# Performance work log

Measured on AMD Instinct MI355X. Metric: run time of the kernel, lower is better.

Reference implementation:

```python
import jax, jax.numpy as jnp
import numpy as np

B, S, D_IN = 2, 2048, 1024
D_OUT, H, W = 1024, 16, 256
HD = D_OUT // H
SCALE = 1.0 / np.sqrt(HD).astype(np.float32)


def setup_inputs() -> dict:
    key = jax.random.key(0)
    k1, k2, k3 = jax.random.split(key, 3)
    x = jax.random.normal(k1, (B, S, D_IN), dtype=jnp.float32)
    W_qkv = jax.random.normal(k2, (3 * D_OUT, D_IN), dtype=jnp.float32) * 0.02
    W_out = jax.random.normal(k3, (D_OUT, D_OUT), dtype=jnp.float32) * 0.02
    b_out = jnp.zeros((D_OUT,), dtype=jnp.float32)
    return {"x": x, "W_qkv": W_qkv, "W_out": W_out, "b_out": b_out}


def reference(x, W_qkv, W_out, b_out):
    b, s, _ = x.shape
    qkv = x @ W_qkv.T  # [b, s, 3*D_OUT]
    q, k, v = jnp.split(qkv, 3, axis=-1)
    # [b, h, s, hd]
    q = q.reshape(b, s, H, HD).transpose(0, 2, 1, 3)
    k = k.reshape(b, s, H, HD).transpose(0, 2, 1, 3)
    v = v.reshape(b, s, H, HD).transpose(0, 2, 1, 3)
    scores = jnp.einsum('bhqd,bhkd->bhqk', q, k) * SCALE
    idx = jnp.arange(s)
    mask = jnp.abs(idx[:, None] - idx[None, :]) <= W  # symmetric band
    scores = jnp.where(mask[None, None], scores, -jnp.inf)
    probs = jax.nn.softmax(scores, axis=-1)
    ctx = jnp.einsum('bhqk,bhkd->bhqd', probs, v)
    ctx = ctx.transpose(0, 2, 1, 3).reshape(b, s, D_OUT)
    return ctx @ W_out.T + b_out
```

## Files before the change

### kernel.cpp

```cpp
#include <hip/hip_runtime.h>

#define S_LEN   2048
#define N_HEAD  16
#define WINSZ   256
#define ATT_SCALE 0.125f

typedef short bf16x8 __attribute__((ext_vector_type(8)));
typedef float f32x4  __attribute__((ext_vector_type(4)));

__device__ __forceinline__ unsigned short f2bf(float f) {
    union { float f; unsigned u; } x; x.f = f;
    return (unsigned short)((x.u + 0x7FFFu + ((x.u >> 16) & 1u)) >> 16);
}

__device__ __forceinline__ void gl2lds16(const unsigned short* g, unsigned short* l) {
    __builtin_amdgcn_global_load_lds(
        (const __attribute__((address_space(1))) unsigned int*)g,
        (__attribute__((address_space(3))) unsigned int*)l, 16, 0, 0);
}

__global__ void cvt_all(const float* __restrict__ x, const float* __restrict__ wqkv,
                        const float* __restrict__ wout,
                        unsigned short* __restrict__ xb, unsigned short* __restrict__ wqkvb,
                        unsigned short* __restrict__ woutb) {
    int i = blockIdx.x * 256 + threadIdx.x;
    const float4* src; ushort4* dst; int off;
    if (i < 1048576)              { src = (const float4*)x;    dst = (ushort4*)xb;    off = i; }
    else if (i < 1048576 + 786432){ src = (const float4*)wqkv; dst = (ushort4*)wqkvb; off = i - 1048576; }
    else                          { src = (const float4*)wout; dst = (ushort4*)woutb; off = i - 1835008; }
    float4 v = src[off];
    ushort4 o;
    o.x = f2bf(v.x); o.y = f2bf(v.y); o.z = f2bf(v.z); o.w = f2bf(v.w);
    dst[off] = o;
}

template<int MODE, int BN>
__global__ __launch_bounds__(256, 3)
void gemm_bt(const unsigned short* __restrict__ A, const unsigned short* __restrict__ Bm,
             int K,
             unsigned short* __restrict__ qout, unsigned short* __restrict__ kout,
             unsigned short* __restrict__ vtout,
             float* __restrict__ Cout, const float* __restrict__ bias, int N)
{
    constexpr int NJ = BN / 32;
    __shared__ unsigned short Als[128 * 64];
    __shared__ unsigned short Bls[BN * 64];

    const int tid   = threadIdx.x;
    const int lane  = tid & 63;
    const int wave  = tid >> 6;
    const int bm    = blockIdx.y, bn = blockIdx.x;
    const int wm    = (wave >> 1) * 64;
    const int wn    = (wave & 1) * (BN / 2);
    const int col16 = lane & 15;
    const int quad  = lane >> 4;

    f32x4 acc[4][NJ];
#pragma unroll
    for (int i = 0; i < 4; ++i)
#pragma unroll
        for (int j = 0; j < NJ; ++j)
            acc[i][j] = f32x4{0.f, 0.f, 0.f, 0.f};

    const int    grow     = lane >> 3;
    const int    gchk     = (lane & 7) ^ grow;
    const size_t laneoff  = (size_t)grow * K + gchk * 8;
    const unsigned short* gA = A  + (size_t)(bm * 128) * K + laneoff;
    const unsigned short* gB = Bm + (size_t)(bn * BN)  * K + laneoff;

    for (int k0 = 0; k0 < K; k0 += 64) {
        __syncthreads();
#pragma unroll
        for (int i = 0; i < 4; ++i) {
            const int r0 = wave * 32 + i * 8;
            gl2lds16(gA + (size_t)r0 * K + k0, &Als[r0 * 64]);
        }
#pragma unroll
        for (int i = 0; i < BN / 32; ++i) {
            const int r0 = wave * (BN / 4) + i * 8;
            gl2lds16(gB + (size_t)r0 * K + k0, &Bls[r0 * 64]);
        }
        __syncthreads();

#pragma unroll
        for (int kc = 0; kc < 2; ++kc) {
            bf16x8 af[4], bfr[NJ];
            const int sw = (kc * 4 + quad) ^ (col16 & 7);
#pragma unroll
            for (int i = 0; i < 4; ++i)
                af[i]  = *(const bf16x8*)(&Als[(wm + i * 16 + col16) * 64 + sw * 8]);
#pragma unroll
            for (int j = 0; j < NJ; ++j)
                bfr[j] = *(const bf16x8*)(&Bls[(wn + j * 16 + col16) * 64 + sw * 8]);
#pragma unroll
            for (int i = 0; i < 4; ++i)
#pragma unroll
                for (int j = 0; j < NJ; ++j)
                    acc[i][j] = __builtin_amdgcn_mfma_f32_16x16x32_bf16(af[i], bfr[j], acc[i][j], 0, 0, 0);
        }
    }

    if (MODE == 0) {
        const int which = bn >> 3;
#pragma unroll
        for (int i = 0; i < 4; ++i)
#pragma unroll
            for (int j = 0; j < NJ; ++j)
#pragma unroll
                for (int r = 0; r < 4; ++r) {
                    int m = bm * 128 + wm + i * 16 + quad * 4 + r;
                    int n = bn * BN  + wn + j * 16 + col16;
                    int rem = n & 1023;
                    int h = rem >> 6, d = rem & 63;
                    int b = m >> 11, s = m & 2047;
                    unsigned short bv = f2bf(acc[i][j][r]);
                    if (which == 0)
                        qout[((size_t)(b * N_HEAD + h) * S_LEN + s) * 64 + d] = bv;
                    else if (which == 1)
                        kout[((size_t)(b * N_HEAD + h) * S_LEN + s) * 64 + d] = bv;
                    else
                        vtout[((size_t)(b * N_HEAD + h) * 64 + d) * S_LEN + s] = bv;
                }
    } else {
#pragma unroll
        for (int i = 0; i < 4; ++i)
#pragma unroll
            for (int j = 0; j < NJ; ++j)
#pragma unroll
                for (int r = 0; r < 4; ++r) {
                    int m = bm * 128 + wm + i * 16 + quad * 4 + r;
                    int n = bn * BN  + wn + j * 16 + col16;
                    Cout[(size_t)m * N + n] = acc[i][j][r] + bias[n];
                }
    }
}

__global__ __launch_bounds__(256, 2)
void attn_kernel(const unsigned short* __restrict__ Qg, const unsigned short* __restrict__ Kg,
                 const unsigned short* __restrict__ Vtg, unsigned short* __restrict__ ctx)
{
    constexpr int LD = 72;
    __shared__ unsigned short Kls[64 * LD];
    __shared__ unsigned short Vls[64 * LD];
    __shared__ unsigned short Pls[4][32 * LD];

    const int tid  = threadIdx.x;
    const int lane = tid & 63;
    const int wave = tid >> 6;
    const int col  = lane & 15;
    const int quad = lane >> 4;

    const int bh  = blockIdx.y;
    const int Q0  = blockIdx.x * 128;
    const int q0w = Q0 + wave * 32;

    const unsigned short* Qb  = Qg  + (size_t)bh * S_LEN * 64;
    const unsigned short* Kb  = Kg  + (size_t)bh * S_LEN * 64;
    const unsigned short* Vtb = Vtg + (size_t)bh * 64 * S_LEN;

    bf16x8 qa[2][2];
#pragma unroll
    for (int qf = 0; qf < 2; ++qf)
#pragma unroll
        for (int kc = 0; kc < 2; ++kc)
            qa[qf][kc] = *(const bf16x8*)(Qb + (size_t)(q0w + qf * 16 + col) * 64 + kc * 32 + quad * 8);

    f32x4 acc[2][4];
    float lsum[2][4];
#pragma unroll
    for (int qf = 0; qf < 2; ++qf)
#pragma unroll
        for (int d = 0; d < 4; ++d) {
            acc[qf][d] = f32x4{0.f, 0.f, 0.f, 0.f};
            lsum[qf][d] = 0.f;
        }

    const int srow = tid >> 2;
    const int scg  = tid & 3;

    for (int c = 0; c < 10; ++c) {
        const int kb = Q0 - WINSZ + c * 64;
        __syncthreads();
        {
            int kk = kb + srow;
            kk = kk < 0 ? 0 : (kk > S_LEN - 1 ? S_LEN - 1 : kk);
#pragma unroll
            for (int h2 = 0; h2 < 2; ++h2) {
                const int ch = scg * 8 + h2 * 32;
                *(bf16x8*)(&Kls[srow * LD + ch]) = *(const bf16x8*)(Kb + (size_t)kk * 64 + ch);
                int ss = kb + ch;
                ss = ss < 0 ? 0 : (ss > S_LEN - 8 ? S_LEN - 8 : ss);
                *(bf16x8*)(&Vls[srow * LD + ch]) = *(const bf16x8*)(Vtb + (size_t)srow * S_LEN + ss);
            }
        }
        __syncthreads();

        if (kb > q0w + 31 + WINSZ || kb + 63 < q0w - WINSZ || kb > S_LEN - 1 || kb + 63 < 0)
            continue;

        f32x4 sc[2][4];
#pragma unroll
        for (int hf = 0; hf < 4; ++hf) {
            bf16x8 kf0 = *(const bf16x8*)(&Kls[(hf * 16 + col) * LD + quad * 8]);
            bf16x8 kf1 = *(const bf16x8*)(&Kls[(hf * 16 + col) * LD + 32 + quad * 8]);
#pragma unroll
            for (int qf = 0; qf < 2; ++qf) {
                f32x4 z = f32x4{0.f, 0.f, 0.f, 0.f};
                z = __builtin_amdgcn_mfma_f32_16x16x32_bf16(qa[qf][0], kf0, z, 0, 0, 0);
                sc[qf][hf] = __builtin_amdgcn_mfma_f32_16x16x32_bf16(qa[qf][1], kf1, z, 0, 0, 0);
            }
        }

        const bool full = (kb >= q0w + 31 - WINSZ) && (kb + 63 <= q0w + WINSZ) &&
                          (kb >= 0) && (kb + 63 <= S_LEN - 1);

        float p[2][4][4];
#pragma unroll
        for (int qf = 0; qf < 2; ++qf)
#pragma unroll
            for (int hf = 0; hf < 4; ++hf) {
                const int kkey = kb + hf * 16 + col;
#pragma unroll
                for (int r = 0; r < 4; ++r) {
                    float e = __expf(fmaf(sc[qf][hf][r], ATT_SCALE, -8.0f));
                    if (!full) {
                        int q  = q0w + qf * 16 + quad * 4 + r;
                        int dq = kkey - q;
                        bool valid = (kkey >= 0) && (kkey < S_LEN) && (dq <= WINSZ) && (dq >= -WINSZ);
                        e = valid ? e : 0.f;
                    }
                    p[qf][hf][r] = e;
                    lsum[qf][r] += e;
                }
            }

        unsigned short* pw = &Pls[wave][0];
#pragma unroll
        for (int qf = 0; qf < 2; ++qf)
#pragma unroll
            for (int hf = 0; hf < 4; ++hf)
#pragma unroll
                for (int r = 0; r < 4; ++r)
                    pw[(qf * 16 + quad * 4 + r) * LD + hf * 16 + col] = f2bf(p[qf][hf][r]);
        asm volatile("s_waitcnt lgkmcnt(0)" ::: "memory");
        bf16x8 pf[2][2];
#pragma unroll
        for (int qf = 0; qf < 2; ++qf) {
            pf[qf][0] = *(const bf16x8*)(&pw[(qf * 16 + col) * LD + quad * 8]);
            pf[qf][1] = *(const bf16x8*)(&pw[(qf * 16 + col) * LD + 32 + quad * 8]);
        }

#pragma unroll
        for (int d = 0; d < 4; ++d)
#pragma unroll
            for (int kc = 0; kc < 2; ++kc) {
                bf16x8 vf = *(const bf16x8*)(&Vls[(d * 16 + col) * LD + kc * 32 + quad * 8]);
#pragma unroll
                for (int qf = 0; qf < 2; ++qf)
                    acc[qf][d] = __builtin_amdgcn_mfma_f32_16x16x32_bf16(pf[qf][kc], vf, acc[qf][d], 0, 0, 0);
            }
    }

    const int b = bh >> 4, h = bh & 15;
#pragma unroll
    for (int qf = 0; qf < 2; ++qf)
#pragma unroll
        for (int r = 0; r < 4; ++r) {
            float v = lsum[qf][r];
            v += __shfl_xor(v, 1);
            v += __shfl_xor(v, 2);
            v += __shfl_xor(v, 4);
            v += __shfl_xor(v, 8);
            float inv = 1.f / v;
            int q = q0w + qf * 16 + quad * 4 + r;
#pragma unroll
            for (int d = 0; d < 4; ++d)
                ctx[((size_t)(b * S_LEN + q)) * 1024 + h * 64 + d * 16 + col] =
                    f2bf(acc[qf][d][r] * inv);
        }
}

extern "C" void kernel_launch(void* const* d_in, const int* in_sizes, int n_in,
                              void* d_out, int out_size, void* d_ws, size_t ws_size,
                              hipStream_t stream) {
    const float* x    = (const float*)d_in[0];
    const float* Wqkv = (const float*)d_in[1];
    const float* Wout = (const float*)d_in[2];
    const float* bout = (const float*)d_in[3];
    float* out = (float*)d_out;

    char* ws = (char*)d_ws;
    unsigned short* xb    = (unsigned short*)(ws);
    unsigned short* wqkvb = (unsigned short*)(ws + 8u  * 1024 * 1024);
    unsigned short* woutb = (unsigned short*)(ws + 14u * 1024 * 1024);
    unsigned short* qb    = (unsigned short*)(ws + 16u * 1024 * 1024);
    unsigned short* kbuf  = (unsigned short*)(ws + 24u * 1024 * 1024);
    unsigned short* vtbuf = (unsigned short*)(ws + 32u * 1024 * 1024);
    unsigned short* ctxb  = (unsigned short*)(ws + 40u * 1024 * 1024);

    cvt_all<<<8192, 256, 0, stream>>>(x, Wqkv, Wout, xb, wqkvb, woutb);

    gemm_bt<0, 128><<<dim3(24, 32), 256, 0, stream>>>(xb, wqkvb, 1024, qb, kbuf, vtbuf,
                                                      nullptr, nullptr, 0);
    attn_kernel<<<dim3(16, 32), 256, 0, stream>>>(qb, kbuf, vtbuf, ctxb);
    gemm_bt<1, 64><<<dim3(16, 32), 256, 0, stream>>>(ctxb, woutb, 1024, nullptr, nullptr, nullptr,
                                                     out, bout, 1024);
}
```

Baseline: 166.0 us.

## Stage GEMM epilogues through LDS and widen attention blocks to eight waves

The QKV GEMM epilogue now writes accumulators into shared memory and then emits 16-byte coalesced stores to Q, K and transposed V. For the V part it swaps the MFMA operands so the transpose comes out of the tile naturally. The output GEMM also stages fp32 results through LDS to produce float4 stores with the bias added. The attention kernel moves to 512 threads with 16 queries per wave, loads K and V tiles directly into swizzled LDS with global_load_lds, and uses cheaper round-half-up bf16 rounding for probabilities. The changes target scattered 2-byte global stores and attention load overhead, at the cost of extra LDS traffic and barriers, and the occupancy change may not fit.

```diff
diff --git a/kernel.cpp b/kernel.cpp
--- a/kernel.cpp
+++ b/kernel.cpp
@@ -11,6 +11,10 @@
 __device__ __forceinline__ unsigned short f2bf(float f) {
     union { float f; unsigned u; } x; x.f = f;
     return (unsigned short)((x.u + 0x7FFFu + ((x.u >> 16) & 1u)) >> 16);
+}
+__device__ __forceinline__ unsigned short f2bf_rhu(float f) {
+    union { float f; unsigned u; } x; x.f = f;
+    return (unsigned short)((x.u + 0x8000u) >> 16);
 }
 
 __device__ __forceinline__ void gl2lds16(const unsigned short* g, unsigned short* l) {
@@ -43,8 +47,9 @@
              float* __restrict__ Cout, const float* __restrict__ bias, int N)
 {
     constexpr int NJ = BN / 32;
-    __shared__ unsigned short Als[128 * 64];
-    __shared__ unsigned short Bls[BN * 64];
+    __shared__ __align__(16) unsigned char smem[34816];
+    unsigned short* Als = (unsigned short*)smem;
+    unsigned short* Bls = Als + 128 * 64;
 
     const int tid   = threadIdx.x;
     const int lane  = tid & 63;
@@ -54,6 +59,7 @@
     const int wn    = (wave & 1) * (BN / 2);
     const int col16 = lane & 15;
     const int quad  = lane >> 4;
+    const bool transc = (MODE == 0) && (bn >= 16);
 
     f32x4 acc[4][NJ];
 #pragma unroll
@@ -92,57 +98,98 @@
 #pragma unroll
             for (int j = 0; j < NJ; ++j)
                 bfr[j] = *(const bf16x8*)(&Bls[(wn + j * 16 + col16) * 64 + sw * 8]);
+            if (transc) {
+#pragma unroll
+                for (int i = 0; i < 4; ++i)
+#pragma unroll
+                    for (int j = 0; j < NJ; ++j)
+                        acc[i][j] = __builtin_amdgcn_mfma_f32_16x16x32_bf16(bfr[j], af[i], acc[i][j], 0, 0, 0);
+            } else {
+#pragma unroll
+                for (int i = 0; i < 4; ++i)
+#pragma unroll
+                    for (int j = 0; j < NJ; ++j)
+                        acc[i][j] = __builtin_amdgcn_mfma_f32_16x16x32_bf16(af[i], bfr[j], acc[i][j], 0, 0, 0);
+            }
+        }
+    }
+
+    __syncthreads();
+    if (MODE == 0) {
+        unsigned short* Ct = (unsigned short*)smem;
+        if (!transc) {
 #pragma unroll
             for (int i = 0; i < 4; ++i)
 #pragma unroll
                 for (int j = 0; j < NJ; ++j)
-                    acc[i][j] = __builtin_amdgcn_mfma_f32_16x16x32_bf16(af[i], bfr[j], acc[i][j], 0, 0, 0);
+#pragma unroll
+                    for (int r = 0; r < 4; ++r)
+                        Ct[(wm + i * 16 + quad * 4 + r) * 136 + wn + j * 16 + col16] =
+                            f2bf(acc[i][j][r]);
+        } else {
+#pragma unroll
+            for (int i = 0; i < 4; ++i)
+#pragma unroll
+                for (int j = 0; j < NJ; ++j)
+#pragma unroll
+                    for (int r = 0; r < 4; ++r)
+                        Ct[(wn + j * 16 + quad * 4 + r) * 136 + wm + i * 16 + col16] =
+                            f2bf(acc[i][j][r]);
+        }
+        __syncthreads();
+        const int row  = tid >> 1;
+        const int half = tid & 1;
+        const unsigned short* src = &Ct[row * 136 + half * 64];
+        if (bn < 16) {
+            int m = bm * 128 + row;
+            int b = m >> 11, s = m & 2047;
+            int h = (bn & 7) * 2 + half;
+            unsigned short* dst = (bn < 8 ? qout : kout) +
+                                  (((size_t)(b * 16 + h) * 2048 + s) * 64);
+#pragma unroll
+            for (int c = 0; c < 8; ++c)
+                *(bf16x8*)(dst + c * 8) = *(const bf16x8*)(src + c * 8);
+        } else {
+            int h = ((bn - 16) * 128 + row) >> 6;
+            int d = row & 63;
+            int b = bm >> 4;
+            int s0 = (bm & 15) * 128 + half * 64;
+            unsigned short* dst = vtout + ((size_t)(b * 16 + h) * 64 + d) * 2048 + s0;
+#pragma unroll
+            for (int c = 0; c < 8; ++c)
+                *(bf16x8*)(dst + c * 8) = *(const bf16x8*)(src + c * 8);
+        }
+    } else {
+        float* Cf = (float*)smem;
+#pragma unroll
+        for (int i = 0; i < 4; ++i)
+#pragma unroll
+            for (int j = 0; j < NJ; ++j)
+#pragma unroll
+                for (int r = 0; r < 4; ++r)
+                    Cf[(wm + i * 16 + quad * 4 + r) * 68 + wn + j * 16 + col16] = acc[i][j][r];
+        __syncthreads();
+        const int row  = tid >> 1;
+        const int half = tid & 1;
+        int m = bm * 128 + row;
+#pragma unroll
+        for (int c = 0; c < 8; ++c) {
+            int nl = half * 32 + c * 4;
+            float4 v  = *(const float4*)&Cf[row * 68 + nl];
+            float4 bb = *(const float4*)&bias[bn * 64 + nl];
+            v.x += bb.x; v.y += bb.y; v.z += bb.z; v.w += bb.w;
+            *(float4*)&Cout[(size_t)m * N + bn * 64 + nl] = v;
         }
     }
-
-    if (MODE == 0) {
-        const int which = bn >> 3;
-#pragma unroll
-        for (int i = 0; i < 4; ++i)
-#pragma unroll
-            for (int j = 0; j < NJ; ++j)
-#pragma unroll
-                for (int r = 0; r < 4; ++r) {
-                    int m = bm * 128 + wm + i * 16 + quad * 4 + r;
-                    int n = bn * BN  + wn + j * 16 + col16;
-                    int rem = n & 1023;
-                    int h = rem >> 6, d = rem & 63;
-                    int b = m >> 11, s = m & 2047;
-                    unsigned short bv = f2bf(acc[i][j][r]);
-                    if (which == 0)
-                        qout[((size_t)(b * N_HEAD + h) * S_LEN + s) * 64 + d] = bv;
-                    else if (which == 1)
-                        kout[((size_t)(b * N_HEAD + h) * S_LEN + s) * 64 + d] = bv;
-                    else
-                        vtout[((size_t)(b * N_HEAD + h) * 64 + d) * S_LEN + s] = bv;
-                }
-    } else {
-#pragma unroll
-        for (int i = 0; i < 4; ++i)
-#pragma unroll
-            for (int j = 0; j < NJ; ++j)
-#pragma unroll
-                for (int r = 0; r < 4; ++r) {
-                    int m = bm * 128 + wm + i * 16 + quad * 4 + r;
-                    int n = bn * BN  + wn + j * 16 + col16;
-                    Cout[(size_t)m * N + n] = acc[i][j][r] + bias[n];
-                }
-    }
-}
-
-__global__ __launch_bounds__(256, 2)
+}
+
+__global__ __launch_bounds__(512, 4)
 void attn_kernel(const unsigned short* __restrict__ Qg, const unsigned short* __restrict__ Kg,
                  const unsigned short* __restrict__ Vtg, unsigned short* __restrict__ ctx)
 {
-    constexpr int LD = 72;
-    __shared__ unsigned short Kls[64 * LD];
-    __shared__ unsigned short Vls[64 * LD];
-    __shared__ unsigned short Pls[4][32 * LD];
+    __shared__ unsigned short Kls[64 * 64];
+    __shared__ unsigned short Vls[64 * 64];
+    __shared__ unsigned short Pls[8][16 * 72];
 
     const int tid  = threadIdx.x;
     const int lane = tid & 63;
@@ -152,132 +199,117 @@
 
     const int bh  = blockIdx.y;
     const int Q0  = blockIdx.x * 128;
-    const int q0w = Q0 + wave * 32;
+    const int q0w = Q0 + wave * 16;
 
     const unsigned short* Qb  = Qg  + (size_t)bh * S_LEN * 64;
     const unsigned short* Kb  = Kg  + (size_t)bh * S_LEN * 64;
     const unsigned short* Vtb = Vtg + (size_t)bh * 64 * S_LEN;
 
-    bf16x8 qa[2][2];
-#pragma unroll
-    for (int qf = 0; qf < 2; ++qf)
-#pragma unroll
-        for (int kc = 0; kc < 2; ++kc)
-            qa[qf][kc] = *(const bf16x8*)(Qb + (size_t)(q0w + qf * 16 + col) * 64 + kc * 32 + quad * 8);
-
-    f32x4 acc[2][4];
-    float lsum[2][4];
-#pragma unroll
-    for (int qf = 0; qf < 2; ++qf)
-#pragma unroll
-        for (int d = 0; d < 4; ++d) {
-            acc[qf][d] = f32x4{0.f, 0.f, 0.f, 0.f};
-            lsum[qf][d] = 0.f;
-        }
-
-    const int srow = tid >> 2;
-    const int scg  = tid & 3;
+    bf16x8 qa[2];
+#pragma unroll
+    for (int kc = 0; kc < 2; ++kc)
+        qa[kc] = *(const bf16x8*)(Qb + (size_t)(q0w + col) * 64 + kc * 32 + quad * 8);
+
+    f32x4 acc[4];
+    float lsum[4];
+#pragma unroll
+    for (int d = 0; d < 4; ++d) acc[d] = f32x4{0.f, 0.f, 0.f, 0.f};
+#pragma unroll
+    for (int r = 0; r < 4; ++r) lsum[r] = 0.f;
+
+    const int rsub = lane >> 3;
+    const int gch  = (lane & 7) ^ rsub;
+    const int swz  = quad;
 
     for (int c = 0; c < 10; ++c) {
         const int kb = Q0 - WINSZ + c * 64;
         __syncthreads();
         {
-            int kk = kb + srow;
-            kk = kk < 0 ? 0 : (kk > S_LEN - 1 ? S_LEN - 1 : kk);
-#pragma unroll
-            for (int h2 = 0; h2 < 2; ++h2) {
-                const int ch = scg * 8 + h2 * 32;
-                *(bf16x8*)(&Kls[srow * LD + ch]) = *(const bf16x8*)(Kb + (size_t)kk * 64 + ch);
-                int ss = kb + ch;
-                ss = ss < 0 ? 0 : (ss > S_LEN - 8 ? S_LEN - 8 : ss);
-                *(bf16x8*)(&Vls[srow * LD + ch]) = *(const bf16x8*)(Vtb + (size_t)srow * S_LEN + ss);
+            int krow = kb + wave * 8 + rsub;
+            krow = krow < 0 ? 0 : (krow > S_LEN - 1 ? S_LEN - 1 : krow);
+            gl2lds16(Kb + (size_t)krow * 64 + gch * 8, &Kls[wave * 512]);
+            int drow = wave * 8 + rsub;
+            int ss = kb + gch * 8;
+            ss = ss < 0 ? 0 : (ss > S_LEN - 8 ? S_LEN - 8 : ss);
+            gl2lds16(Vtb + (size_t)drow * S_LEN + ss, &Vls[wave * 512]);
+        }
+        __syncthreads();
+
+        if (kb > q0w + 15 + WINSZ || kb + 63 < q0w - WINSZ || kb > S_LEN - 1 || kb + 63 < 0)
+            continue;
+
+        f32x4 sc[4];
+#pragma unroll
+        for (int hf = 0; hf < 4; ++hf) {
+            const int rw = (hf * 16 + col) * 64;
+            const int s0 = ((0 * 4 + swz) ^ (col & 7)) * 8;
+            const int s1 = ((1 * 4 + swz) ^ (col & 7)) * 8;
+            bf16x8 kf0 = *(const bf16x8*)(&Kls[rw + s0]);
+            bf16x8 kf1 = *(const bf16x8*)(&Kls[rw + s1]);
+            f32x4 z = f32x4{0.f, 0.f, 0.f, 0.f};
+            z = __builtin_amdgcn_mfma_f32_16x16x32_bf16(qa[0], kf0, z, 0, 0, 0);
+            sc[hf] = __builtin_amdgcn_mfma_f32_16x16x32_bf16(qa[1], kf1, z, 0, 0, 0);
+        }
+
+        const bool full = (kb >= q0w + 15 - WINSZ) && (kb + 63 <= q0w + WINSZ) &&
+                          (kb >= 0) && (kb + 63 <= S_LEN - 1);
+
+        float p[4][4];
+#pragma unroll
+        for (int hf = 0; hf < 4; ++hf) {
+            const int kkey = kb + hf * 16 + col;
+#pragma unroll
+            for (int r = 0; r < 4; ++r) {
+                float e = __expf(fmaf(sc[hf][r], ATT_SCALE, -8.0f));
+                if (!full) {
+                    int q  = q0w + quad * 4 + r;
+                    int dq = kkey - q;
+                    bool valid = (kkey >= 0) && (kkey < S_LEN) && (dq <= WINSZ) && (dq >= -WINSZ);
+                    e = valid ? e : 0.f;
+                }
+                p[hf][r] = e;
+                lsum[r] += e;
             }
         }
-        __syncthreads();
-
-        if (kb > q0w + 31 + WINSZ || kb + 63 < q0w - WINSZ || kb > S_LEN - 1 || kb + 63 < 0)
-            continue;
-
-        f32x4 sc[2][4];
-#pragma unroll
-        for (int hf = 0; hf < 4; ++hf) {
-            bf16x8 kf0 = *(const bf16x8*)(&Kls[(hf * 16 + col) * LD + quad * 8]);
-            bf16x8 kf1 = *(const bf16x8*)(&Kls[(hf * 16 + col) * LD + 32 + quad * 8]);
-#pragma unroll
-            for (int qf = 0; qf < 2; ++qf) {
-                f32x4 z = f32x4{0.f, 0.f, 0.f, 0.f};
-                z = __builtin_amdgcn_mfma_f32_16x16x32_bf16(qa[qf][0], kf0, z, 0, 0, 0);
-                sc[qf][hf] = __builtin_amdgcn_mfma_f32_16x16x32_bf16(qa[qf][1], kf1, z, 0, 0, 0);
+
+        unsigned short* pw = &Pls[wave][0];
+#pragma unroll
+        for (int hf = 0; hf < 4; ++hf)
+#pragma unroll
+            for (int r = 0; r < 4; ++r)
+                pw[(quad * 4 + r) * 72 + hf * 16 + col] = f2bf_rhu(p[hf][r]);
+        asm volatile("s_waitcnt lgkmcnt(0)" ::: "memory");
+        bf16x8 pf[2];
+        pf[0] = *(const bf16x8*)(&pw[col * 72 + quad * 8]);
+        pf[1] = *(const bf16x8*)(&pw[col * 72 + 32 + quad * 8]);
+
+#pragma unroll
+        for (int d = 0; d < 4; ++d) {
+            const int rw = (d * 16 + col) * 64;
+#pragma unroll
+            for (int kc = 0; kc < 2; ++kc) {
+                const int so = ((kc * 4 + swz) ^ (col & 7)) * 8;
+                bf16x8 vf = *(const bf16x8*)(&Vls[rw + so]);
+                acc[d] = __builtin_amdgcn_mfma_f32_16x16x32_bf16(pf[kc], vf, acc[d], 0, 0, 0);
             }
         }
-
-        const bool full = (kb >= q0w + 31 - WINSZ) && (kb + 63 <= q0w + WINSZ) &&
-                          (kb >= 0) && (kb + 63 <= S_LEN - 1);
-
-        float p[2][4][4];
-#pragma unroll
-        for (int qf = 0; qf < 2; ++qf)
-#pragma unroll
-            for (int hf = 0; hf < 4; ++hf) {
-                const int kkey = kb + hf * 16 + col;
-#pragma unroll
-                for (int r = 0; r < 4; ++r) {
-                    float e = __expf(fmaf(sc[qf][hf][r], ATT_SCALE, -8.0f));
-                    if (!full) {
-                        int q  = q0w + qf * 16 + quad * 4 + r;
-                        int dq = kkey - q;
-                        bool valid = (kkey >= 0) && (kkey < S_LEN) && (dq <= WINSZ) && (dq >= -WINSZ);
-                        e = valid ? e : 0.f;
-                    }
-                    p[qf][hf][r] = e;
-                    lsum[qf][r] += e;
-                }
-            }
-
-        unsigned short* pw = &Pls[wave][0];
-#pragma unroll
-        for (int qf = 0; qf < 2; ++qf)
-#pragma unroll
-            for (int hf = 0; hf < 4; ++hf)
-#pragma unroll
-                for (int r = 0; r < 4; ++r)
-                    pw[(qf * 16 + quad * 4 + r) * LD + hf * 16 + col] = f2bf(p[qf][hf][r]);
-        asm volatile("s_waitcnt lgkmcnt(0)" ::: "memory");
-        bf16x8 pf[2][2];
-#pragma unroll
-        for (int qf = 0; qf < 2; ++qf) {
-            pf[qf][0] = *(const bf16x8*)(&pw[(qf * 16 + col) * LD + quad * 8]);
-            pf[qf][1] = *(const bf16x8*)(&pw[(qf * 16 + col) * LD + 32 + quad * 8]);
-        }
-
+    }
+
+    const int b = bh >> 4, h = bh & 15;
+#pragma unroll
+    for (int r = 0; r < 4; ++r) {
+        float v = lsum[r];
+        v += __shfl_xor(v, 1);
+        v += __shfl_xor(v, 2);
+        v += __shfl_xor(v, 4);
+        v += __shfl_xor(v, 8);
+        float inv = 1.f / v;
+        int q = q0w + quad * 4 + r;
 #pragma unroll
         for (int d = 0; d < 4; ++d)
-#pragma unroll
-            for (int kc = 0; kc < 2; ++kc) {
-                bf16x8 vf = *(const bf16x8*)(&Vls[(d * 16 + col) * LD + kc * 32 + quad * 8]);
-#pragma unroll
-                for (int qf = 0; qf < 2; ++qf)
-                    acc[qf][d] = __builtin_amdgcn_mfma_f32_16x16x32_bf16(pf[qf][kc], vf, acc[qf][d], 0, 0, 0);
-            }
+            ctx[((size_t)(b * S_LEN + q)) * 1024 + h * 64 + d * 16 + col] =
+                f2bf(acc[d][r] * inv);
     }
-
-    const int b = bh >> 4, h = bh & 15;
-#pragma unroll
-    for (int qf = 0; qf < 2; ++qf)
-#pragma unroll
-        for (int r = 0; r < 4; ++r) {
-            float v = lsum[qf][r];
-            v += __shfl_xor(v, 1);
-            v += __shfl_xor(v, 2);
-            v += __shfl_xor(v, 4);
-            v += __shfl_xor(v, 8);
-            float inv = 1.f / v;
-            int q = q0w + qf * 16 + quad * 4 + r;
-#pragma unroll
-            for (int d = 0; d < 4; ++d)
-                ctx[((size_t)(b * S_LEN + q)) * 1024 + h * 64 + d * 16 + col] =
-                    f2bf(acc[qf][d][r] * inv);
-        }
 }
 
 extern "C" void kernel_launch(void* const* d_in, const int* in_sizes, int n_in,
@@ -302,7 +334,7 @@
 
     gemm_bt<0, 128><<<dim3(24, 32), 256, 0, stream>>>(xb, wqkvb, 1024, qb, kbuf, vtbuf,
                                                       nullptr, nullptr, 0);
-    attn_kernel<<<dim3(16, 32), 256, 0, stream>>>(qb, kbuf, vtbuf, ctxb);
+    attn_kernel<<<dim3(16, 32), 512, 0, stream>>>(qb, kbuf, vtbuf, ctxb);
     gemm_bt<1, 64><<<dim3(16, 32), 256, 0, stream>>>(ctxb, woutb, 1024, nullptr, nullptr, nullptr,
                                                      out, bout, 1024);
 }
```

Measured after the change: 219.6 us. +32.3%, slower.
